# Kernel tuning notes

Measured on AMD Instinct MI355X. Metric: run time of the kernel, lower is better.

Reference implementation:

```python
import jax, jax.numpy as jnp
import numpy as np

D_MODEL = 512
MAX_LEN = 30000          # m/z grid size: MAX_MZ(3000) * spectrum_reso(10)
SPECTRUM_RESO = 10.0
BATCH = 1024
N_PEAKS = 500            # config.MAX_NUM_PEAK
MAX_MZ = 3000.0


def _make_pe(max_len, d_model):
    # sinusoidal table [max_len+1, d_model]; row 0 zeroed (padding peak)
    position = jnp.arange(max_len + 1, dtype=jnp.float32)[:, None]
    div_term = jnp.exp(jnp.arange(0, d_model, 2, dtype=jnp.float32)
                       * (-jnp.log(jnp.float32(10000.0)) / d_model))
    pe = jnp.zeros((max_len + 1, d_model), dtype=jnp.float32)
    pe = pe.at[:, 0::2].set(jnp.sin(position * div_term))
    pe = pe.at[:, 1::2].set(jnp.cos(position * div_term))
    pe = pe.at[0, :].set(0.0)
    return pe


def setup_inputs() -> dict:
    key = jax.random.key(0)
    k1, k2 = jax.random.split(key)
    # m/z locations in [0, 3000) so ceil(loc * reso) indexes pe in-range
    peaks_location = jax.random.uniform(k1, (BATCH, N_PEAKS), dtype=jnp.float32) * MAX_MZ
    peaks_intensity = jax.random.uniform(k2, (BATCH, N_PEAKS), dtype=jnp.float32)
    pe = _make_pe(MAX_LEN, D_MODEL)
    return {"peaks_location": peaks_location,
            "peaks_intensity": peaks_intensity,
            "pe": pe}


def reference(peaks_location, peaks_intensity, pe):
    # fused gather-scale-reduce: sum_n pe[ceil(loc*reso)] * intensity
    idx = jnp.ceil(peaks_location * SPECTRUM_RESO).astype(jnp.int32)  # [B, N]
    gathered = pe[idx]                                               # [B, N, D]
    return jnp.einsum("bnd,bn->bd", gathered, peaks_intensity)       # [B, D]
```

## Files before the change

### kernel.cpp

```cpp
#include <hip/hip_runtime.h>
#include <hip/hip_bf16.h>
#include <math.h>

#define D_MODEL 512
#define N_PEAKS 500
#define BATCH   1024
#define BLOCK   256

__global__ __launch_bounds__(BLOCK)
void SpectrumEncoding_84164179132426_kernel(const float* __restrict__ loc,
                                            const float* __restrict__ inten,
                                            float* __restrict__ out) {
    __shared__ float2 s_iw[N_PEAKS];

    const int b = blockIdx.x;
    const int t = threadIdx.x;

    for (int n = t; n < N_PEAKS; n += BLOCK) {
        float l    = loc[b * N_PEAKS + n];
        float idxf = ceilf(l * 10.0f);
        float w    = inten[b * N_PEAKS + n];
        s_iw[n] = make_float2(idxf, (idxf == 0.0f) ? 0.0f : w);
    }
    __syncthreads();

    const float c  = -logf(10000.0f) / (float)D_MODEL;
    const float wk = expf((float)(2 * t) * c);

    float acc_s = 0.0f, acc_c = 0.0f;

#pragma unroll 4
    for (int n = 0; n < N_PEAKS; ++n) {
        const float2 iw  = s_iw[n];
        const float  ang = iw.x * wk;
        const float  s   = __sinf(ang);
        const float  cc  = __cosf(ang);
        acc_s = fmaf(iw.y, s,  acc_s);
        acc_c = fmaf(iw.y, cc, acc_c);
    }

    *(float2*)(out + b * D_MODEL + 2 * t) = make_float2(acc_s, acc_c);
}

extern "C" void kernel_launch(void* const* d_in, const int* in_sizes, int n_in,
                              void* d_out, int out_size, void* d_ws, size_t ws_size,
                              hipStream_t stream) {
    const float* loc   = (const float*)d_in[0];
    const float* inten = (const float*)d_in[1];
    float*       out   = (float*)d_out;

    SpectrumEncoding_84164179132426_kernel<<<BATCH, BLOCK, 0, stream>>>(loc, inten, out);
}
```

Measured before the change: 37.12 us.

## Replace per-peak sin/cos with fixed-point phase lookup into shared sine table

Each thread's frequency becomes a 32-bit fixed-point phase increment, so the phase for a peak is an integer multiply with wraparound. Sin/cos then come from a 4096-entry shared-memory table rounded to the nearest entry, replacing the transcendental instructions in the inner loop. The cost is per-block table construction with full-precision sinf/cosf, an extra 32KB of LDS per block that may lower occupancy, scattered LDS reads that can bank-conflict, and quantization error of about one table step in phase.

After: 43.19 us. 16.4% more time.

```diff
diff --git a/kernel.cpp b/kernel.cpp
--- a/kernel.cpp
+++ b/kernel.cpp
@@ -6,37 +6,48 @@
 #define N_PEAKS 500
 #define BATCH   1024
 #define BLOCK   256
+#define TBITS   12
+#define TSIZE   (1 << TBITS)
 
 __global__ __launch_bounds__(BLOCK)
 void SpectrumEncoding_84164179132426_kernel(const float* __restrict__ loc,
                                             const float* __restrict__ inten,
                                             float* __restrict__ out) {
-    __shared__ float2 s_iw[N_PEAKS];
+    __shared__ float2 s_cis[TSIZE];
+    __shared__ uint2  s_iw[N_PEAKS];
 
     const int b = blockIdx.x;
     const int t = threadIdx.x;
+
+    for (int j = t; j < TSIZE; j += BLOCK) {
+        float a = (float)j * (6.28318530717958647693f / (float)TSIZE);
+        s_cis[j] = make_float2(sinf(a), cosf(a));
+    }
 
     for (int n = t; n < N_PEAKS; n += BLOCK) {
         float l    = loc[b * N_PEAKS + n];
         float idxf = ceilf(l * 10.0f);
         float w    = inten[b * N_PEAKS + n];
-        s_iw[n] = make_float2(idxf, (idxf == 0.0f) ? 0.0f : w);
+        unsigned int idx = (unsigned int)idxf;
+        s_iw[n] = make_uint2(idx, __float_as_uint(idx == 0u ? 0.0f : w));
     }
     __syncthreads();
 
-    const float c  = -logf(10000.0f) / (float)D_MODEL;
-    const float wk = expf((float)(2 * t) * c);
+    const double cd = -log(10000.0) / (double)D_MODEL;
+    const double fk = exp((double)(2 * t) * cd) / (2.0 * M_PI);
+    const unsigned int Pk = (unsigned int)llrint(fk * 4294967296.0);
 
     float acc_s = 0.0f, acc_c = 0.0f;
 
 #pragma unroll 4
     for (int n = 0; n < N_PEAKS; ++n) {
-        const float2 iw  = s_iw[n];
-        const float  ang = iw.x * wk;
-        const float  s   = __sinf(ang);
-        const float  cc  = __cosf(ang);
-        acc_s = fmaf(iw.y, s,  acc_s);
-        acc_c = fmaf(iw.y, cc, acc_c);
+        const uint2 iw = s_iw[n];
+        const unsigned int x = iw.x * Pk;
+        const unsigned int j = (x + (1u << (31 - TBITS))) >> (32 - TBITS);
+        const float2 sc = s_cis[j];
+        const float  w  = __uint_as_float(iw.y);
+        acc_s = fmaf(w, sc.x, acc_s);
+        acc_c = fmaf(w, sc.y, acc_c);
     }
 
     *(float2*)(out + b * D_MODEL + 2 * t) = make_float2(acc_s, acc_c);
```
